# Performance work log

Measured on AMD Instinct MI355X. Metric: run time of the kernel, lower is better.

## Reference

```python
import jax, jax.numpy as jnp
import numpy as np

COMMITMENT_COST = 0.25


def setup_inputs() -> dict:
    key = jax.random.key(0)
    k1, k2 = jax.random.split(key)
    B, C, H, W, D = 8, 64, 32, 32, 32
    NUM_EMB = 512
    x = jax.random.normal(k1, (B, C, H, W, D), dtype=jnp.float32)
    # torch init: uniform(-1/num_embeddings, 1/num_embeddings)
    codebook = jax.random.uniform(k2, (NUM_EMB, C), dtype=jnp.float32,
                                  minval=-1.0 / NUM_EMB, maxval=1.0 / NUM_EMB)
    return {"x": x, "codebook": codebook}


def reference(x, codebook):
    B, C, H, W, D = x.shape
    # [B,C,H,W,D] -> [N, C] with N = B*H*W*D
    flat = jnp.transpose(x, (0, 2, 3, 4, 1)).reshape(-1, C)
    # squared L2 distances to every codebook entry: [N, num_embeddings]
    dist = (jnp.sum(flat * flat, axis=1, keepdims=True)
            - 2.0 * flat @ codebook.T
            + jnp.sum(codebook * codebook, axis=1))
    idx = jnp.argmin(dist, axis=1)                     # [N]
    # one-hot @ codebook  ==  gather (same math, efficient form)
    quant_flat = codebook[idx]                          # [N, C]
    quant = jnp.transpose(quant_flat.reshape(B, H, W, D, C), (0, 4, 1, 2, 3))
    e_loss = jnp.mean((jax.lax.stop_gradient(quant) - x) ** 2)
    q_loss = jnp.mean((quant - jax.lax.stop_gradient(x)) ** 2)
    loss = q_loss + COMMITMENT_COST * e_loss
    # straight-through estimator
    quant_st = x + jax.lax.stop_gradient(quant - x)
    return quant_st, loss
```

## Files before the change

kernel.cpp:

```cpp
#include <hip/hip_runtime.h>
#include <cstdint>
#include <cstddef>

#define SPATIAL   32768
#define CHANNELS  64
#define NUM_EMB   512
#define NPOS      262144
#define OUT_ELEMS 16777216
#define BLOCK     256
#define LOSS_SCALE (1.25f / 16777216.0f)

#define NT_TOTAL     32
#define NT_PER_CHUNK 8
#define NCHUNK       4
#define CHUNK_BYTES  16384

typedef __attribute__((ext_vector_type(8))) short bf16x8;
typedef __attribute__((ext_vector_type(4))) float f32x4;

union b8u { int i[4]; bf16x8 v; };
union fiu { float f; unsigned u; };

__device__ __forceinline__ short f2bf_rne(float f) {
    fiu v; v.f = f;
    unsigned r = v.u + 0x7fffu + ((v.u >> 16) & 1u);
    return (short)(r >> 16);
}

__global__ void vq_prep(const float* __restrict__ cb,
                        short* __restrict__ cbfrag,
                        float* __restrict__ cbn,
                        float* __restrict__ loss_slot) {
    int e = blockIdx.x * blockDim.x + threadIdx.x;
    if (e == 0) *loss_slot = 0.0f;
    if (e < NUM_EMB) {
        const int nt  = e >> 4;
        const int col = e & 15;
        float s = 0.0f;
#pragma unroll
        for (int q = 0; q < 4; ++q) {
#pragma unroll
            for (int j = 0; j < 8; ++j) {
                float v0 = cb[e * CHANNELS + q * 8 + j];
                float v1 = cb[e * CHANNELS + 32 + q * 8 + j];
                cbfrag[nt * 1024 + (q * 16 + col) * 8 + j]       = f2bf_rne(v0);
                cbfrag[nt * 1024 + 512 + (q * 16 + col) * 8 + j] = f2bf_rne(v1);
            }
        }
#pragma unroll
        for (int c = 0; c < CHANNELS; ++c) {
            float v = cb[e * CHANNELS + c];
            s = __builtin_fmaf(v, v, s);
        }
        cbn[e] = -0.5f * s;
    }
}

__global__ __launch_bounds__(BLOCK) void vq_main(
    const float* __restrict__ x,
    const float* __restrict__ cb,
    const short* __restrict__ cbfrag,
    const float* __restrict__ cbn,
    float* __restrict__ out,
    float* __restrict__ loss_slot) {
#pragma clang fp contract(off)
    __shared__ __align__(16) char smem[32768];
    __shared__ int   cand[BLOCK];
    __shared__ float wsum[4];

    short* stageS = (short*)smem;
    float* qbuf   = (float*)smem;

    const int tid  = threadIdx.x;
    const int wave = tid >> 6, lane = tid & 63;
    const int q    = lane >> 4, col = lane & 15;

    const int blockPos = blockIdx.x * BLOCK;
    const int b     = blockPos >> 15;
    const int sbase = blockPos & 32767;
    const float* xb = x + (size_t)b * (CHANNELS * SPATIAL);
    const int wbase = sbase + wave * 64;

    {
#pragma unroll
        for (int rd = 0; rd < 4; ++rd) {
            const int off = rd * 4096 + wave * 1024;
            const unsigned* g = (const unsigned*)((const char*)cbfrag + off + lane * 16);
            unsigned* l = (unsigned*)(smem + off);
            __builtin_amdgcn_global_load_lds(
                (const __attribute__((address_space(1))) unsigned*)g,
                (__attribute__((address_space(3))) unsigned*)l, 16, 0, 0);
        }
    }

    b8u A[4][2];
#pragma unroll
    for (int t = 0; t < 4; ++t) {
        const unsigned* pu = (const unsigned*)xb + (wbase + t * 16 + col);
#pragma unroll
        for (int kh = 0; kh < 2; ++kh) {
#pragma unroll
            for (int jj = 0; jj < 4; ++jj) {
                unsigned u0 = pu[(size_t)(kh * 32 + q * 8 + 2 * jj + 0) * SPATIAL];
                unsigned u1 = pu[(size_t)(kh * 32 + q * 8 + 2 * jj + 1) * SPATIAL];
                A[t][kh].i[jj] = __builtin_amdgcn_perm(u1, u0, 0x07060302u);
            }
        }
    }

    float m[4][4];
#pragma unroll
    for (int t = 0; t < 4; ++t)
#pragma unroll
        for (int r = 0; r < 4; ++r) m[t][r] = -3.4e38f;

    const unsigned MASK = 0xFFFFFE00u;
    const int encBase = 511 - col;

    __syncthreads();

#pragma unroll 1
    for (int c = 0; c < NCHUNK; ++c) {
        const int buf = c & 1;
        if (c + 1 < NCHUNK) {
#pragma unroll
            for (int rd = 0; rd < 4; ++rd) {
                const int off = rd * 4096 + wave * 1024;
                const unsigned* g = (const unsigned*)
                    ((const char*)cbfrag + (c + 1) * CHUNK_BYTES + off + lane * 16);
                unsigned* l = (unsigned*)(smem + (buf ^ 1) * CHUNK_BYTES + off);
                __builtin_amdgcn_global_load_lds(
                    (const __attribute__((address_space(1))) unsigned*)g,
                    (__attribute__((address_space(3))) unsigned*)l, 16, 0, 0);
            }
        }
#pragma unroll
        for (int k = 0; k < NT_PER_CHUNK; ++k) {
            const int nt = c * NT_PER_CHUNK + k;
            const int e0 = nt * 16;
            const short* sb = stageS + buf * (CHUNK_BYTES / 2) + k * 1024 + lane * 8;
            bf16x8 B0 = *(const bf16x8*)sb;
            bf16x8 B1 = *(const bf16x8*)(sb + 512);
            float cn = cbn[e0 + col];
            f32x4 ci = {cn, cn, cn, cn};
            const unsigned enc = (unsigned)(encBase - e0);
#pragma unroll
            for (int t = 0; t < 4; ++t) {
                f32x4 acc = __builtin_amdgcn_mfma_f32_16x16x32_bf16(A[t][0].v, B0, ci, 0, 0, 0);
                acc = __builtin_amdgcn_mfma_f32_16x16x32_bf16(A[t][1].v, B1, acc, 0, 0, 0);
#pragma unroll
                for (int r = 0; r < 4; ++r) {
                    fiu p; p.f = acc[r];
                    p.u = (p.u & MASK) | enc;
                    m[t][r] = fmaxf(m[t][r], p.f);
                }
            }
        }
        __syncthreads();
    }

#pragma unroll
    for (int t = 0; t < 4; ++t) {
#pragma unroll
        for (int r = 0; r < 4; ++r) {
            float v = m[t][r];
#pragma unroll
            for (int d = 1; d < 16; d <<= 1)
                v = fmaxf(v, __shfl_xor(v, d, 64));
            if (col == 0) {
                fiu p; p.f = v;
                cand[wave * 64 + t * 16 + q * 4 + r] = 511 - (int)(p.u & 511u);
            }
        }
    }
    __syncthreads();

    const int pos = tid;
    const int gr  = tid >> 3;
    const int gl  = tid & 7;
    const float* pxb = xb + (sbase + pos);
    float* opb = out + (size_t)b * (CHANNELS * SPATIAL) + (sbase + pos);
    float lsum = 0.0f;

#pragma unroll 1
    for (int cc = 0; cc < 2; ++cc) {
#pragma unroll
        for (int rd = 0; rd < 8; ++rd) {
            const int r   = rd * 32 + gr;
            const int row = cand[r];
            f32x4 v = *((const f32x4*)(cb + (size_t)row * CHANNELS + cc * 32) + gl);
            const int lsw = gl ^ (r & 7);
            *((f32x4*)(qbuf + r * 32 + lsw * 4)) = v;
        }
        __syncthreads();
        const float* px = pxb + (size_t)(cc * 32) * SPATIAL;
        float* op = opb + (size_t)(cc * 32) * SPATIAL;
#pragma unroll
        for (int j = 0; j < 8; ++j) {
            const int jsw = j ^ (pos & 7);
            f32x4 qq = *((const f32x4*)(qbuf + pos * 32 + jsw * 4));
#pragma unroll
            for (int k = 0; k < 4; ++k) {
                const int ch = j * 4 + k;
                float xv = px[(size_t)ch * SPATIAL];
                float t2 = qq[k] - xv;
                op[(size_t)ch * SPATIAL] = xv + t2;
                lsum = __builtin_fmaf(t2, t2, lsum);
            }
        }
        if (cc == 0) __syncthreads();
    }

#pragma unroll
    for (int off = 32; off > 0; off >>= 1) lsum += __shfl_down(lsum, off, 64);
    if (lane == 0) wsum[wave] = lsum;
    __syncthreads();
    if (tid == 0) {
        float bs = (wsum[0] + wsum[1]) + (wsum[2] + wsum[3]);
        atomicAdd(loss_slot, bs * LOSS_SCALE);
    }
}

extern "C" void kernel_launch(void* const* d_in, const int* in_sizes, int n_in,
                              void* d_out, int out_size, void* d_ws, size_t ws_size,
                              hipStream_t stream) {
    const float* x  = (const float*)d_in[0];
    const float* cb = (const float*)d_in[1];
    float* out = (float*)d_out;
    short* cbfrag = (short*)d_ws;
    float* cbn    = (float*)(cbfrag + NUM_EMB * CHANNELS);
    float* loss_slot = out + OUT_ELEMS;

    vq_prep<<<2, 256, 0, stream>>>(cb, cbfrag, cbn, loss_slot);
    vq_main<<<NPOS / BLOCK, BLOCK, 0, stream>>>(x, cb, cbfrag, cbn, out, loss_slot);
}
```

Before: 141.6 us.

## Load full codebook to LDS once, swap MFMA operands, split x loads

Loads the whole 32KB bf16 codebook fragment into LDS in one shot instead of double-buffered chunks, removing the per-chunk barriers. It swaps the MFMA operand order so codebook entries land on rows, so each lane keeps one running max per tile and the final reduction needs only two cross-lane shuffles instead of a 16-way reduction per row. The x fragment loads for the second half of the tiles are issued early and converted only after the first half's compute, overlapping global latency with MFMA work. This trades higher LDS use (32KB per block, possibly lower occupancy) and more live registers for fewer syncs and shuffles.

```diff
diff --git a/kernel.cpp b/kernel.cpp
--- a/kernel.cpp
+++ b/kernel.cpp
@@ -9,11 +9,6 @@
 #define OUT_ELEMS 16777216
 #define BLOCK     256
 #define LOSS_SCALE (1.25f / 16777216.0f)
-
-#define NT_TOTAL     32
-#define NT_PER_CHUNK 8
-#define NCHUNK       4
-#define CHUNK_BYTES  16384
 
 typedef __attribute__((ext_vector_type(8))) short bf16x8;
 typedef __attribute__((ext_vector_type(4))) float f32x4;
@@ -81,96 +76,118 @@
     const float* xb = x + (size_t)b * (CHANNELS * SPATIAL);
     const int wbase = sbase + wave * 64;
 
-    {
-#pragma unroll
-        for (int rd = 0; rd < 4; ++rd) {
-            const int off = rd * 4096 + wave * 1024;
-            const unsigned* g = (const unsigned*)((const char*)cbfrag + off + lane * 16);
-            unsigned* l = (unsigned*)(smem + off);
-            __builtin_amdgcn_global_load_lds(
-                (const __attribute__((address_space(1))) unsigned*)g,
-                (__attribute__((address_space(3))) unsigned*)l, 16, 0, 0);
-        }
-    }
-
-    b8u A[4][2];
+#pragma unroll
+    for (int rd = 0; rd < 8; ++rd) {
+        const int off = rd * 4096 + wave * 1024;
+        __builtin_amdgcn_global_load_lds(
+            (const __attribute__((address_space(1))) unsigned*)
+                ((const char*)cbfrag + off + lane * 16),
+            (__attribute__((address_space(3))) unsigned*)(smem + off), 16, 0, 0);
+    }
+    __builtin_amdgcn_sched_barrier(0);
+
+    unsigned r01[2][2][4][2], r23[2][2][4][2];
+#pragma unroll
+    for (int t = 0; t < 2; ++t) {
+        const unsigned* pu = (const unsigned*)xb + (wbase + t * 16 + col);
+#pragma unroll
+        for (int kh = 0; kh < 2; ++kh)
+#pragma unroll
+            for (int jj = 0; jj < 4; ++jj) {
+                r01[t][kh][jj][0] = pu[(size_t)(kh * 32 + q * 8 + 2 * jj + 0) * SPATIAL];
+                r01[t][kh][jj][1] = pu[(size_t)(kh * 32 + q * 8 + 2 * jj + 1) * SPATIAL];
+            }
+    }
+#pragma unroll
+    for (int t = 0; t < 2; ++t) {
+        const unsigned* pu = (const unsigned*)xb + (wbase + 32 + t * 16 + col);
+#pragma unroll
+        for (int kh = 0; kh < 2; ++kh)
+#pragma unroll
+            for (int jj = 0; jj < 4; ++jj) {
+                r23[t][kh][jj][0] = pu[(size_t)(kh * 32 + q * 8 + 2 * jj + 0) * SPATIAL];
+                r23[t][kh][jj][1] = pu[(size_t)(kh * 32 + q * 8 + 2 * jj + 1) * SPATIAL];
+            }
+    }
+    __builtin_amdgcn_sched_barrier(0);
+
+    b8u A01[2][2];
+#pragma unroll
+    for (int t = 0; t < 2; ++t)
+#pragma unroll
+        for (int kh = 0; kh < 2; ++kh)
+#pragma unroll
+            for (int jj = 0; jj < 4; ++jj)
+                A01[t][kh].i[jj] = __builtin_amdgcn_perm(
+                    r01[t][kh][jj][1], r01[t][kh][jj][0], 0x07060302u);
+
+    __builtin_amdgcn_sched_barrier(0);
+    __builtin_amdgcn_s_barrier();
+    __builtin_amdgcn_sched_barrier(0);
+
+    float mt[4];
+#pragma unroll
+    for (int t = 0; t < 4; ++t) mt[t] = -3.4e38f;
+    const unsigned MASK = 0xFFFFFE00u;
+
+#pragma unroll 2
+    for (int nt = 0; nt < 32; ++nt) {
+        const short* sb = stageS + nt * 1024 + (lane << 3);
+        bf16x8 CB0 = *(const bf16x8*)sb;
+        bf16x8 CB1 = *(const bf16x8*)(sb + 512);
+        f32x4 civ  = *(const f32x4*)(cbn + nt * 16 + (q << 2));
+        const unsigned encq = (unsigned)(511 - nt * 16 - (q << 2));
+#pragma unroll
+        for (int tt = 0; tt < 2; ++tt) {
+            f32x4 acc = __builtin_amdgcn_mfma_f32_16x16x32_bf16(CB0, A01[tt][0].v, civ, 0, 0, 0);
+            acc = __builtin_amdgcn_mfma_f32_16x16x32_bf16(CB1, A01[tt][1].v, acc, 0, 0, 0);
+#pragma unroll
+            for (int r = 0; r < 4; ++r) {
+                fiu p; p.f = acc[r];
+                p.u = (p.u & MASK) | (encq - r);
+                mt[tt] = fmaxf(mt[tt], p.f);
+            }
+        }
+    }
+
+    b8u A23[2][2];
+#pragma unroll
+    for (int t = 0; t < 2; ++t)
+#pragma unroll
+        for (int kh = 0; kh < 2; ++kh)
+#pragma unroll
+            for (int jj = 0; jj < 4; ++jj)
+                A23[t][kh].i[jj] = __builtin_amdgcn_perm(
+                    r23[t][kh][jj][1], r23[t][kh][jj][0], 0x07060302u);
+
+#pragma unroll 2
+    for (int nt = 0; nt < 32; ++nt) {
+        const short* sb = stageS + nt * 1024 + (lane << 3);
+        bf16x8 CB0 = *(const bf16x8*)sb;
+        bf16x8 CB1 = *(const bf16x8*)(sb + 512);
+        f32x4 civ  = *(const f32x4*)(cbn + nt * 16 + (q << 2));
+        const unsigned encq = (unsigned)(511 - nt * 16 - (q << 2));
+#pragma unroll
+        for (int tt = 0; tt < 2; ++tt) {
+            f32x4 acc = __builtin_amdgcn_mfma_f32_16x16x32_bf16(CB0, A23[tt][0].v, civ, 0, 0, 0);
+            acc = __builtin_amdgcn_mfma_f32_16x16x32_bf16(CB1, A23[tt][1].v, acc, 0, 0, 0);
+#pragma unroll
+            for (int r = 0; r < 4; ++r) {
+                fiu p; p.f = acc[r];
+                p.u = (p.u & MASK) | (encq - r);
+                mt[2 + tt] = fmaxf(mt[2 + tt], p.f);
+            }
+        }
+    }
+
 #pragma unroll
     for (int t = 0; t < 4; ++t) {
-        const unsigned* pu = (const unsigned*)xb + (wbase + t * 16 + col);
-#pragma unroll
-        for (int kh = 0; kh < 2; ++kh) {
-#pragma unroll
-            for (int jj = 0; jj < 4; ++jj) {
-                unsigned u0 = pu[(size_t)(kh * 32 + q * 8 + 2 * jj + 0) * SPATIAL];
-                unsigned u1 = pu[(size_t)(kh * 32 + q * 8 + 2 * jj + 1) * SPATIAL];
-                A[t][kh].i[jj] = __builtin_amdgcn_perm(u1, u0, 0x07060302u);
-            }
-        }
-    }
-
-    float m[4][4];
-#pragma unroll
-    for (int t = 0; t < 4; ++t)
-#pragma unroll
-        for (int r = 0; r < 4; ++r) m[t][r] = -3.4e38f;
-
-    const unsigned MASK = 0xFFFFFE00u;
-    const int encBase = 511 - col;
-
-    __syncthreads();
-
-#pragma unroll 1
-    for (int c = 0; c < NCHUNK; ++c) {
-        const int buf = c & 1;
-        if (c + 1 < NCHUNK) {
-#pragma unroll
-            for (int rd = 0; rd < 4; ++rd) {
-                const int off = rd * 4096 + wave * 1024;
-                const unsigned* g = (const unsigned*)
-                    ((const char*)cbfrag + (c + 1) * CHUNK_BYTES + off + lane * 16);
-                unsigned* l = (unsigned*)(smem + (buf ^ 1) * CHUNK_BYTES + off);
-                __builtin_amdgcn_global_load_lds(
-                    (const __attribute__((address_space(1))) unsigned*)g,
-                    (__attribute__((address_space(3))) unsigned*)l, 16, 0, 0);
-            }
-        }
-#pragma unroll
-        for (int k = 0; k < NT_PER_CHUNK; ++k) {
-            const int nt = c * NT_PER_CHUNK + k;
-            const int e0 = nt * 16;
-            const short* sb = stageS + buf * (CHUNK_BYTES / 2) + k * 1024 + lane * 8;
-            bf16x8 B0 = *(const bf16x8*)sb;
-            bf16x8 B1 = *(const bf16x8*)(sb + 512);
-            float cn = cbn[e0 + col];
-            f32x4 ci = {cn, cn, cn, cn};
-            const unsigned enc = (unsigned)(encBase - e0);
-#pragma unroll
-            for (int t = 0; t < 4; ++t) {
-                f32x4 acc = __builtin_amdgcn_mfma_f32_16x16x32_bf16(A[t][0].v, B0, ci, 0, 0, 0);
-                acc = __builtin_amdgcn_mfma_f32_16x16x32_bf16(A[t][1].v, B1, acc, 0, 0, 0);
-#pragma unroll
-                for (int r = 0; r < 4; ++r) {
-                    fiu p; p.f = acc[r];
-                    p.u = (p.u & MASK) | enc;
-                    m[t][r] = fmaxf(m[t][r], p.f);
-                }
-            }
-        }
-        __syncthreads();
-    }
-
-#pragma unroll
-    for (int t = 0; t < 4; ++t) {
-#pragma unroll
-        for (int r = 0; r < 4; ++r) {
-            float v = m[t][r];
-#pragma unroll
-            for (int d = 1; d < 16; d <<= 1)
-                v = fmaxf(v, __shfl_xor(v, d, 64));
-            if (col == 0) {
-                fiu p; p.f = v;
-                cand[wave * 64 + t * 16 + q * 4 + r] = 511 - (int)(p.u & 511u);
-            }
+        float v = mt[t];
+        v = fmaxf(v, __shfl_xor(v, 16, 64));
+        v = fmaxf(v, __shfl_xor(v, 32, 64));
+        if (lane < 16) {
+            fiu p; p.f = v;
+            cand[wave * 64 + t * 16 + lane] = 511 - (int)(p.u & 511u);
         }
     }
     __syncthreads();
```

Measured after the change: 136.4 us. 3.7% less time.
